# Kernel optimization log

Measured on AMD Instinct MI355X. Metric: run time of the kernel, lower is better.

The kernel has to match this reference:

```python
import jax
import jax.numpy as jnp
from jax import lax
import numpy as np

NUM_OUTPUT_POINTS = 2048
NUM_NEIGHBORS = 32


def setup_inputs() -> dict:
    key = jax.random.key(0)
    k1, k2 = jax.random.split(key)
    coordinates = jax.random.normal(k1, (8, 8192, 3), dtype=jnp.float32)
    features = jax.random.normal(k2, (8, 8192, 128), dtype=jnp.float32)
    return {"coordinates": coordinates, "features": features}


def farthest_point_sample(coords, num_output_points):
    """Deterministic FPS (first point = index 0). coords: (B, N, D) -> idx (B, M) int32."""
    B, N, D = coords.shape

    def step(carry, _):
        dist, farthest = carry  # (B, N), (B,)
        centroid = jnp.take_along_axis(coords, farthest[:, None, None], axis=1)  # (B,1,D)
        cur = jnp.linalg.norm(coords - centroid, axis=-1)  # (B, N), L2 norm
        dist = jnp.minimum(dist, cur)
        new_far = jnp.argmax(dist, axis=-1).astype(jnp.int32)
        return (dist, new_far), farthest

    init = (jnp.full((B, N), 1e10, coords.dtype), jnp.zeros((B,), jnp.int32))
    _, idx = lax.scan(step, init, None, length=num_output_points)  # (M, B)
    return idx.T  # (B, M)


def knn_point(num_neighbors, coords, centers):
    """coords (B,N,D), centers (B,M,D) -> (B,M,K) indices of nearest neighbors (L2)."""
    # squared distances via expansion (avoids (B,M,N,D) diff tensor)
    c2 = jnp.sum(centers * centers, axis=-1, keepdims=True)        # (B,M,1)
    p2 = jnp.sum(coords * coords, axis=-1)[:, None, :]             # (B,1,N)
    d2 = c2 + p2 - 2.0 * jnp.einsum('bmd,bnd->bmn', centers, coords)
    _, nbr_idx = lax.top_k(-d2, num_neighbors)                     # smallest distances
    return nbr_idx


def _gather_points(points, idx):
    """points (B,N,C), idx (B,...) -> (B,...,C)."""
    return jax.vmap(lambda p, i: p[i])(points, idx)


def reference(coordinates, features):
    fps_idx = farthest_point_sample(coordinates, NUM_OUTPUT_POINTS)      # (B, M)
    out_coordinates = _gather_points(coordinates, fps_idx)               # (B, M, D)
    nbr_idx = knn_point(NUM_NEIGHBORS, coordinates, out_coordinates)     # (B, M, K)
    group_features = _gather_points(features, nbr_idx)                   # (B, M, K, C)
    out_features = jnp.mean(group_features, axis=2)                      # (B, M, C)
    return out_coordinates, out_features
```

## Files before the change

### kernel.cpp

```cpp
#include <hip/hip_runtime.h>

typedef unsigned int u32;
typedef unsigned long long u64;
typedef float f32x2 __attribute__((ext_vector_type(2)));

#define BB 8
#define NN 8192
#define MM 2048
#define KK 32
#define CC 128

#define FPS_T 512
#define FPS_PAIRS 8

template <int Ctrl, int RowMask>
__device__ __forceinline__ int dpp_mov(int x) {
  return __builtin_amdgcn_update_dpp(x, x, Ctrl, RowMask, 0xf, false);
}
template <int Ctrl, int RowMask>
__device__ __forceinline__ u32 dpp_scan_add(u32 x) {
  return x + (u32)__builtin_amdgcn_update_dpp(0, (int)x, Ctrl, RowMask, 0xf, false);
}

__device__ __forceinline__ float wave_max63(float v) {
  v = fmaxf(v, __int_as_float(dpp_mov<0x111, 0xf>(__float_as_int(v))));
  v = fmaxf(v, __int_as_float(dpp_mov<0x112, 0xf>(__float_as_int(v))));
  v = fmaxf(v, __int_as_float(dpp_mov<0x114, 0xf>(__float_as_int(v))));
  v = fmaxf(v, __int_as_float(dpp_mov<0x118, 0xf>(__float_as_int(v))));
  v = fmaxf(v, __int_as_float(dpp_mov<0x142, 0xa>(__float_as_int(v))));
  v = fmaxf(v, __int_as_float(dpp_mov<0x143, 0xc>(__float_as_int(v))));
  return v;
}

__device__ __forceinline__ u32 wave_minu63(u32 v) {
  u32 o;
  o = (u32)dpp_mov<0x111, 0xf>((int)v); v = o < v ? o : v;
  o = (u32)dpp_mov<0x112, 0xf>((int)v); v = o < v ? o : v;
  o = (u32)dpp_mov<0x114, 0xf>((int)v); v = o < v ? o : v;
  o = (u32)dpp_mov<0x118, 0xf>((int)v); v = o < v ? o : v;
  o = (u32)dpp_mov<0x142, 0xa>((int)v); v = o < v ? o : v;
  o = (u32)dpp_mov<0x143, 0xc>((int)v); v = o < v ? o : v;
  return v;
}

__device__ __forceinline__ u32 wave_scan_incl(u32 x) {
  x = dpp_scan_add<0x111, 0xf>(x);
  x = dpp_scan_add<0x112, 0xf>(x);
  x = dpp_scan_add<0x114, 0xf>(x);
  x = dpp_scan_add<0x118, 0xf>(x);
  x = dpp_scan_add<0x142, 0xa>(x);
  x = dpp_scan_add<0x143, 0xc>(x);
  return x;
}

#define PK_ADD(d, a, b) asm("v_pk_add_f32 %0, %1, %2" : "=v"(d) : "v"(a), "v"(b))
#define PK_MUL(d, a, b) asm("v_pk_mul_f32 %0, %1, %2" : "=v"(d) : "v"(a), "v"(b))

__global__ __launch_bounds__(FPS_T, 1)
void fps_kernel(const float* __restrict__ coords, float* __restrict__ out_coords) {
  const int b = blockIdx.x;
  const int t = threadIdx.x;
  const float* cb = coords + (size_t)b * NN * 3;

  __shared__ float s_x[NN], s_y[NN], s_z[NN];
  __shared__ float s_gpart[FPS_T / 64];
  __shared__ u32 s_ipart[FPS_T / 64];

  f32x2 x[FPS_PAIRS], y[FPS_PAIRS], z[FPS_PAIRS], d2m[FPS_PAIRS];
#pragma unroll
  for (int k = 0; k < FPS_PAIRS; ++k) {
    const int p0 = t + (2 * k) * FPS_T;
    const int p1 = t + (2 * k + 1) * FPS_T;
    x[k].x = cb[p0 * 3 + 0]; x[k].y = cb[p1 * 3 + 0];
    y[k].x = cb[p0 * 3 + 1]; y[k].y = cb[p1 * 3 + 1];
    z[k].x = cb[p0 * 3 + 2]; z[k].y = cb[p1 * 3 + 2];
    d2m[k].x = 1e20f; d2m[k].y = 1e20f;
    s_x[p0] = x[k].x; s_x[p1] = x[k].y;
    s_y[p0] = y[k].x; s_y[p1] = y[k].y;
    s_z[p0] = z[k].x; s_z[p1] = z[k].y;
  }

  if (t == 0) {
    out_coords[(size_t)(b * MM) * 3 + 0] = cb[0];
    out_coords[(size_t)(b * MM) * 3 + 1] = cb[1];
    out_coords[(size_t)(b * MM) * 3 + 2] = cb[2];
  }
  float cx = cb[0], cy = cb[1], cz = cb[2];

  for (int it = 1; it < MM; ++it) {
    const f32x2 ncx = {-cx, -cx}, ncy = {-cy, -cy}, ncz = {-cz, -cz};
    f32x2 bv = {-1.0f, -1.0f};
#pragma unroll
    for (int k = 0; k < FPS_PAIRS; ++k) {
      f32x2 dx, dy, dz, t0, t1, t2, d2;
      PK_ADD(dx, x[k], ncx);
      PK_ADD(dy, y[k], ncy);
      PK_ADD(dz, z[k], ncz);
      PK_MUL(t0, dx, dx);
      PK_MUL(t1, dy, dy);
      PK_ADD(t0, t0, t1);
      PK_MUL(t2, dz, dz);
      PK_ADD(d2, t0, t2);
      d2m[k].x = fminf(d2m[k].x, d2.x);
      d2m[k].y = fminf(d2m[k].y, d2.y);
      bv.x = fmaxf(bv.x, d2m[k].x);
      bv.y = fmaxf(bv.y, d2m[k].y);
    }
    const float bestv = fmaxf(bv.x, bv.y);

    const float wv = wave_max63(bestv);
    if ((t & 63) == 63) s_gpart[t >> 6] = wv;
    __syncthreads();
    float gmax = s_gpart[0];
#pragma unroll
    for (int w = 1; w < FPS_T / 64; ++w) gmax = fmaxf(gmax, s_gpart[w]);

    float lo_f;
    if (!(gmax > 0.0f)) {
      lo_f = 0.0f;
    } else {
      const float s = __fsqrt_rn(gmax);
      const float sp = __int_as_float(__float_as_int(s) - 1);
      const double mid = 0.5 * ((double)s + (double)sp);
      const double lod = mid * mid;
      float c = (float)lod;
      if ((double)c < lod) c = __int_as_float(__float_as_int(c) + 1);
      lo_f = c;
    }

    u32 mi = 0xFFFFFFFFu;
    if (bestv >= lo_f) {
#pragma unroll
      for (int k = 0; k < FPS_PAIRS; ++k) {
        const u32 p0 = (u32)(t + (2 * k) * FPS_T);
        const u32 p1 = (u32)(t + (2 * k + 1) * FPS_T);
        if (d2m[k].x >= lo_f && p0 < mi) mi = p0;
        if (d2m[k].y >= lo_f && p1 < mi) mi = p1;
      }
    }
    const u32 wi = wave_minu63(mi);
    if ((t & 63) == 63) s_ipart[t >> 6] = wi;
    __syncthreads();
    u32 widx = s_ipart[0];
#pragma unroll
    for (int w = 1; w < FPS_T / 64; ++w)
      widx = s_ipart[w] < widx ? s_ipart[w] : widx;

    cx = s_x[widx]; cy = s_y[widx]; cz = s_z[widx];
    if (t == (it & (FPS_T - 1))) {
      float* oc = out_coords + ((size_t)b * MM + it) * 3;
      oc[0] = cx; oc[1] = cy; oc[2] = cz;
    }
  }
}

__global__ __launch_bounds__(256, 4)
void knn_mean_kernel(const float* __restrict__ coords,
                     const float* __restrict__ feats,
                     const float* __restrict__ out_coords,
                     float* __restrict__ out_feats) {
  const int q = blockIdx.x;
  const int b = q >> 11;
  const int t = threadIdx.x;
  const float* cb = coords + (size_t)b * NN * 3;

  const float cx = out_coords[(size_t)q * 3 + 0];
  const float cy = out_coords[(size_t)q * 3 + 1];
  const float cz = out_coords[(size_t)q * 3 + 2];
  const float c2 = __fadd_rn(__fadd_rn(__fmul_rn(cx, cx), __fmul_rn(cy, cy)),
                             __fmul_rn(cz, cz));

  u32 D[32];
  const float* tb = cb + t * 96;
#pragma unroll
  for (int ch = 0; ch < 8; ++ch) {
    const float4 q0 = *(const float4*)(tb + ch * 12 + 0);
    const float4 q1 = *(const float4*)(tb + ch * 12 + 4);
    const float4 q2 = *(const float4*)(tb + ch * 12 + 8);
    const float pxs[4] = {q0.x, q0.w, q1.z, q2.y};
    const float pys[4] = {q0.y, q1.x, q1.w, q2.z};
    const float pzs[4] = {q0.z, q1.y, q2.x, q2.w};
#pragma unroll
    for (int kk = 0; kk < 4; ++kk) {
      const int j = ch * 4 + kk;
      const float px = pxs[kk], py = pys[kk], pz = pzs[kk];
      const float p2 = __fadd_rn(__fadd_rn(__fmul_rn(px, px), __fmul_rn(py, py)),
                                 __fmul_rn(pz, pz));
      const float dot = __fmaf_rn(cz, pz, __fmaf_rn(cy, py, __fmul_rn(cx, px)));
      const float d2 = __fsub_rn(__fadd_rn(c2, p2), __fadd_rn(dot, dot));
      u32 ub = __float_as_uint(d2);
      ub ^= (((u32)((int)ub >> 31)) | 0x80000000u);
      D[j] = ub;
    }
  }

  __shared__ u32 s_hist[4096];
  __shared__ u32 s_wsum[4];
  __shared__ u32 s_bin, s_r, s_full;
  __shared__ u32 s_cnt;
  __shared__ int s_nbr[KK];
  __shared__ float s_sum[CC];

  const int w = t >> 6;
  u64 hi = 0;
  u32 k_rem = KK;
  u64 thr = 0;
  bool done = false;

  constexpr int SHIFT[4] = {33, 22, 11, 0};
  constexpr int SBITS[4] = {45, 33, 22, 11};

#pragma unroll
  for (int p = 0; p < 4; ++p) {
    if (!done) {
      const uint4 z4 = {0u, 0u, 0u, 0u};
#pragma unroll
      for (int i = 0; i < 4; ++i) *(uint4*)&s_hist[t * 16 + i * 4] = z4;
      __syncthreads();

#pragma unroll
      for (int j = 0; j < 32; ++j) {
        const u64 key = ((u64)D[j] << 13) | (u32)(t * 32 + j);
        if ((key >> SBITS[p]) == hi)
          atomicAdd(&s_hist[(u32)(key >> SHIFT[p]) & 4095u], 1u);
      }
      __syncthreads();

      const uint4 h0 = *(const uint4*)&s_hist[t * 16 + 0];
      const uint4 h1 = *(const uint4*)&s_hist[t * 16 + 4];
      const uint4 h2 = *(const uint4*)&s_hist[t * 16 + 8];
      const uint4 h3 = *(const uint4*)&s_hist[t * 16 + 12];
      const u32 ls = h0.x + h0.y + h0.z + h0.w + h1.x + h1.y + h1.z + h1.w +
                     h2.x + h2.y + h2.z + h2.w + h3.x + h3.y + h3.z + h3.w;
      const u32 incl = wave_scan_incl(ls);
      if ((t & 63) == 63) s_wsum[w] = incl;
      __syncthreads();
      u32 base = 0;
      if (w > 0) base += s_wsum[0];
      if (w > 1) base += s_wsum[1];
      if (w > 2) base += s_wsum[2];
      const u32 pre_grp = base + incl - ls;

      if (pre_grp < k_rem && k_rem <= pre_grp + ls) {
        const u32 hh[16] = {h0.x, h0.y, h0.z, h0.w, h1.x, h1.y, h1.z, h1.w,
                            h2.x, h2.y, h2.z, h2.w, h3.x, h3.y, h3.z, h3.w};
        u32 c = pre_grp;
#pragma unroll
        for (int i = 0; i < 16; ++i) {
          const u32 h = hh[i];
          if (k_rem > c && k_rem <= c + h) {
            s_bin = (u32)(t * 16 + i);
            s_r = k_rem - c;
            s_full = (k_rem - c == h) ? 1u : 0u;
          }
          c += h;
        }
      }
      __syncthreads();

      const u32 bin = s_bin;
      const u32 r = s_r;
      const u32 fullf = s_full;
      hi = (hi << (SBITS[p] - SHIFT[p])) | bin;
      if (fullf) {
        thr = (SHIFT[p] > 0)
                  ? ((hi << SHIFT[p]) | ((1ULL << SHIFT[p]) - 1ULL))
                  : hi;
        done = true;
      } else {
        k_rem = r;
      }
    }
  }

  if (t == 0) s_cnt = 0;
  __syncthreads();
#pragma unroll
  for (int j = 0; j < 32; ++j) {
    const u64 key = ((u64)D[j] << 13) | (u32)(t * 32 + j);
    if (key <= thr) {
      const u32 pos = atomicAdd(&s_cnt, 1u);
      s_nbr[pos] = t * 32 + j;
    }
  }
  __syncthreads();

  const int c = t & (CC - 1);
  const int half = t >> 7;
  const float* fb = feats + (size_t)b * NN * CC;
  float s = 0.0f;
#pragma unroll
  for (int k = 0; k < 16; ++k) {
    const int p = s_nbr[half * 16 + k];
    s = __fadd_rn(s, fb[(size_t)p * CC + c]);
  }
  if (half == 1) s_sum[c] = s;
  __syncthreads();
  if (half == 0) {
    const float tot = __fadd_rn(s, s_sum[c]);
    out_feats[(size_t)q * CC + c] = tot * 0.03125f;
  }
}

extern "C" void kernel_launch(void* const* d_in, const int* in_sizes, int n_in,
                              void* d_out, int out_size, void* d_ws, size_t ws_size,
                              hipStream_t stream) {
  const float* coords = (const float*)d_in[0];
  const float* feats  = (const float*)d_in[1];
  float* out_coords = (float*)d_out;
  float* out_feats  = (float*)d_out + (size_t)BB * MM * 3;

  fps_kernel<<<BB, FPS_T, 0, stream>>>(coords, out_coords);
  knn_mean_kernel<<<BB * MM, 256, 0, stream>>>(coords, feats, out_coords,
                                               out_feats);
}
```

Measured before the change: 2.499 ms.

## Spatially sort FPS points into Morton cells and skip threads/waves via bounding spheres

Before the FPS loop, the kernel bins each batch's points into a 16^3 Morton-ordered grid with a shared-memory histogram and prefix scan, so every thread holds 16 spatially adjacent points. It then builds a bounding sphere per thread and per wave. Each iteration tests the new centroid against these spheres, using conservative rounding factors, and skips the distance update when no point in the sphere can get a smaller min-distance. The argmax tie-break now compares square roots and uses the original point indices, meant to match the reference's L2-norm argmax. This adds setup cost and divergence, and exact equivalence depends on the rounding bounds.

```diff
diff --git a/kernel.cpp b/kernel.cpp
--- a/kernel.cpp
+++ b/kernel.cpp
@@ -2,7 +2,6 @@
 
 typedef unsigned int u32;
 typedef unsigned long long u64;
-typedef float f32x2 __attribute__((ext_vector_type(2)));
 
 #define BB 8
 #define NN 8192
@@ -11,7 +10,11 @@
 #define CC 128
 
 #define FPS_T 512
-#define FPS_PAIRS 8
+#define FPS_P 16
+#define NCELL 4096
+
+#define C_DOWN 0.9999961853027344f
+#define C_UP   1.0000038146972656f
 
 template <int Ctrl, int RowMask>
 __device__ __forceinline__ int dpp_mov(int x) {
@@ -31,7 +34,15 @@
   v = fmaxf(v, __int_as_float(dpp_mov<0x143, 0xc>(__float_as_int(v))));
   return v;
 }
-
+__device__ __forceinline__ float wave_min63f(float v) {
+  v = fminf(v, __int_as_float(dpp_mov<0x111, 0xf>(__float_as_int(v))));
+  v = fminf(v, __int_as_float(dpp_mov<0x112, 0xf>(__float_as_int(v))));
+  v = fminf(v, __int_as_float(dpp_mov<0x114, 0xf>(__float_as_int(v))));
+  v = fminf(v, __int_as_float(dpp_mov<0x118, 0xf>(__float_as_int(v))));
+  v = fminf(v, __int_as_float(dpp_mov<0x142, 0xa>(__float_as_int(v))));
+  v = fminf(v, __int_as_float(dpp_mov<0x143, 0xc>(__float_as_int(v))));
+  return v;
+}
 __device__ __forceinline__ u32 wave_minu63(u32 v) {
   u32 o;
   o = (u32)dpp_mov<0x111, 0xf>((int)v); v = o < v ? o : v;
@@ -42,7 +53,6 @@
   o = (u32)dpp_mov<0x143, 0xc>((int)v); v = o < v ? o : v;
   return v;
 }
-
 __device__ __forceinline__ u32 wave_scan_incl(u32 x) {
   x = dpp_scan_add<0x111, 0xf>(x);
   x = dpp_scan_add<0x112, 0xf>(x);
@@ -52,32 +62,106 @@
   x = dpp_scan_add<0x143, 0xc>(x);
   return x;
 }
-
-#define PK_ADD(d, a, b) asm("v_pk_add_f32 %0, %1, %2" : "=v"(d) : "v"(a), "v"(b))
-#define PK_MUL(d, a, b) asm("v_pk_mul_f32 %0, %1, %2" : "=v"(d) : "v"(a), "v"(b))
+__device__ __forceinline__ float rl63(float v) {
+  return __uint_as_float((u32)__builtin_amdgcn_readlane(__float_as_int(v), 63));
+}
+
+__device__ __forceinline__ u32 spread4(u32 a) {
+  return (a & 1u) | ((a & 2u) << 2) | ((a & 4u) << 4) | ((a & 8u) << 6);
+}
+__device__ __forceinline__ u32 cell_of(float x, float y, float z) {
+  const u32 qx = (u32)(int)fminf(fmaxf((x + 6.0f) * 1.3333334f, 0.0f), 15.0f);
+  const u32 qy = (u32)(int)fminf(fmaxf((y + 6.0f) * 1.3333334f, 0.0f), 15.0f);
+  const u32 qz = (u32)(int)fminf(fmaxf((z + 6.0f) * 1.3333334f, 0.0f), 15.0f);
+  return spread4(qx) | (spread4(qy) << 1) | (spread4(qz) << 2);
+}
 
 __global__ __launch_bounds__(FPS_T, 1)
 void fps_kernel(const float* __restrict__ coords, float* __restrict__ out_coords) {
-  const int b = blockIdx.x;
-  const int t = threadIdx.x;
+  const int b = blockIdx.x, t = threadIdx.x, w = t >> 6, lane = t & 63;
   const float* cb = coords + (size_t)b * NN * 3;
 
   __shared__ float s_x[NN], s_y[NN], s_z[NN];
+  __shared__ u32 s_sidx[NN];
+  __shared__ u32 s_hist[NCELL];
   __shared__ float s_gpart[FPS_T / 64];
   __shared__ u32 s_ipart[FPS_T / 64];
-
-  f32x2 x[FPS_PAIRS], y[FPS_PAIRS], z[FPS_PAIRS], d2m[FPS_PAIRS];
-#pragma unroll
-  for (int k = 0; k < FPS_PAIRS; ++k) {
-    const int p0 = t + (2 * k) * FPS_T;
-    const int p1 = t + (2 * k + 1) * FPS_T;
-    x[k].x = cb[p0 * 3 + 0]; x[k].y = cb[p1 * 3 + 0];
-    y[k].x = cb[p0 * 3 + 1]; y[k].y = cb[p1 * 3 + 1];
-    z[k].x = cb[p0 * 3 + 2]; z[k].y = cb[p1 * 3 + 2];
-    d2m[k].x = 1e20f; d2m[k].y = 1e20f;
-    s_x[p0] = x[k].x; s_x[p1] = x[k].y;
-    s_y[p0] = y[k].x; s_y[p1] = y[k].y;
-    s_z[p0] = z[k].x; s_z[p1] = z[k].y;
+  __shared__ u32 s_wsum[FPS_T / 64];
+
+  u32 cell[FPS_P];
+  {
+    float lx[FPS_P], ly[FPS_P], lz[FPS_P];
+#pragma unroll
+    for (int j = 0; j < FPS_P; ++j) {
+      const int p = t + j * FPS_T;
+      lx[j] = cb[p * 3 + 0]; ly[j] = cb[p * 3 + 1]; lz[j] = cb[p * 3 + 2];
+      s_x[p] = lx[j]; s_y[p] = ly[j]; s_z[p] = lz[j];
+    }
+#pragma unroll
+    for (int i = 0; i < NCELL / FPS_T; ++i) s_hist[t + i * FPS_T] = 0u;
+    __syncthreads();
+#pragma unroll
+    for (int j = 0; j < FPS_P; ++j) {
+      cell[j] = cell_of(lx[j], ly[j], lz[j]);
+      atomicAdd(&s_hist[cell[j]], 1u);
+    }
+  }
+  __syncthreads();
+
+  {
+    u32 h[8], ls = 0;
+#pragma unroll
+    for (int i = 0; i < 8; ++i) { h[i] = s_hist[t * 8 + i]; ls += h[i]; }
+    const u32 incl = wave_scan_incl(ls);
+    if (lane == 63) s_wsum[w] = incl;
+    __syncthreads();
+    u32 base = 0;
+#pragma unroll
+    for (int w2 = 0; w2 < FPS_T / 64; ++w2) base += (w2 < w) ? s_wsum[w2] : 0u;
+    u32 run = base + incl - ls;
+#pragma unroll
+    for (int i = 0; i < 8; ++i) { const u32 hv = h[i]; s_hist[t * 8 + i] = run; run += hv; }
+  }
+  __syncthreads();
+
+#pragma unroll
+  for (int j = 0; j < FPS_P; ++j) {
+    const u32 pos = atomicAdd(&s_hist[cell[j]], 1u);
+    s_sidx[pos] = (u32)(t + j * FPS_T);
+  }
+  __syncthreads();
+
+  float x[FPS_P], y[FPS_P], z[FPS_P], d2m[FPS_P];
+  u32 idx[FPS_P];
+  float ccx, ccy, ccz, Rup;
+  {
+    float sx = 0.f, sy = 0.f, sz = 0.f;
+#pragma unroll
+    for (int j = 0; j < FPS_P; ++j) {
+      idx[j] = s_sidx[t * FPS_P + j];
+      x[j] = s_x[idx[j]]; y[j] = s_y[idx[j]]; z[j] = s_z[idx[j]];
+      d2m[j] = 1e20f;
+      sx += x[j]; sy += y[j]; sz += z[j];
+    }
+    ccx = sx * 0.0625f; ccy = sy * 0.0625f; ccz = sz * 0.0625f;
+    float r2 = 0.f;
+#pragma unroll
+    for (int j = 0; j < FPS_P; ++j) {
+      const float dx = x[j] - ccx, dy = y[j] - ccy, dz = z[j] - ccz;
+      r2 = fmaxf(r2, dx * dx + dy * dy + dz * dz);
+    }
+    Rup = __fsqrt_rn(r2) * C_UP + 1e-30f;
+  }
+
+  float wcx, wcy, wcz, wR;
+  {
+    const float lx = rl63(wave_min63f(ccx - Rup)), hx = rl63(wave_max63(ccx + Rup));
+    const float ly = rl63(wave_min63f(ccy - Rup)), hy = rl63(wave_max63(ccy + Rup));
+    const float lz = rl63(wave_min63f(ccz - Rup)), hz = rl63(wave_max63(ccz + Rup));
+    wcx = (lx + hx) * 0.5f; wcy = (ly + hy) * 0.5f; wcz = (lz + hz) * 0.5f;
+    const float ddx = ccx - wcx, ddy = ccy - wcy, ddz = ccz - wcz;
+    const float dr = __fsqrt_rn(ddx * ddx + ddy * ddy + ddz * ddz) * C_UP + Rup;
+    wR = rl63(wave_max63(dr)) * C_UP + 1e-30f;
   }
 
   if (t == 0) {
@@ -86,65 +170,63 @@
     out_coords[(size_t)(b * MM) * 3 + 2] = cb[2];
   }
   float cx = cb[0], cy = cb[1], cz = cb[2];
+  float bestv = 1e20f;
+  float wbest = 1e20f;
 
   for (int it = 1; it < MM; ++it) {
-    const f32x2 ncx = {-cx, -cx}, ncy = {-cy, -cy}, ncz = {-cz, -cz};
-    f32x2 bv = {-1.0f, -1.0f};
-#pragma unroll
-    for (int k = 0; k < FPS_PAIRS; ++k) {
-      f32x2 dx, dy, dz, t0, t1, t2, d2;
-      PK_ADD(dx, x[k], ncx);
-      PK_ADD(dy, y[k], ncy);
-      PK_ADD(dz, z[k], ncz);
-      PK_MUL(t0, dx, dx);
-      PK_MUL(t1, dy, dy);
-      PK_ADD(t0, t0, t1);
-      PK_MUL(t2, dz, dz);
-      PK_ADD(d2, t0, t2);
-      d2m[k].x = fminf(d2m[k].x, d2.x);
-      d2m[k].y = fminf(d2m[k].y, d2.y);
-      bv.x = fmaxf(bv.x, d2m[k].x);
-      bv.y = fmaxf(bv.y, d2m[k].y);
-    }
-    const float bestv = fmaxf(bv.x, bv.y);
-
-    const float wv = wave_max63(bestv);
-    if ((t & 63) == 63) s_gpart[t >> 6] = wv;
+    const float wdx = __fsub_rn(wcx, cx), wdy = __fsub_rn(wcy, cy), wdz = __fsub_rn(wcz, cz);
+    const float wd2 = __fadd_rn(__fadd_rn(__fmul_rn(wdx, wdx), __fmul_rn(wdy, wdy)),
+                                __fmul_rn(wdz, wdz));
+    const float wlc = __fsub_rn(__fmul_rn(__fsqrt_rn(wd2), C_DOWN), wR);
+    const bool wskip = (wlc > 0.0f) &&
+                       (__fmul_rn(__fmul_rn(wlc, wlc), C_DOWN) >= wbest);
+    if (!wskip) {
+      const float tdx = __fsub_rn(ccx, cx), tdy = __fsub_rn(ccy, cy), tdz = __fsub_rn(ccz, cz);
+      const float td2 = __fadd_rn(__fadd_rn(__fmul_rn(tdx, tdx), __fmul_rn(tdy, tdy)),
+                                  __fmul_rn(tdz, tdz));
+      const float tlc = __fsub_rn(__fmul_rn(__fsqrt_rn(td2), C_DOWN), Rup);
+      const bool tskip = (tlc > 0.0f) &&
+                         (__fmul_rn(__fmul_rn(tlc, tlc), C_DOWN) >= bestv);
+      if (!tskip) {
+        float bv = -1.0f;
+#pragma unroll
+        for (int j = 0; j < FPS_P; ++j) {
+          const float dx = __fsub_rn(x[j], cx);
+          const float dy = __fsub_rn(y[j], cy);
+          const float dz = __fsub_rn(z[j], cz);
+          const float d2 = __fadd_rn(__fadd_rn(__fmul_rn(dx, dx), __fmul_rn(dy, dy)),
+                                     __fmul_rn(dz, dz));
+          const float nd = fminf(d2m[j], d2);
+          d2m[j] = nd;
+          bv = fmaxf(bv, nd);
+        }
+        bestv = bv;
+      }
+      const float wv = wave_max63(bestv);
+      if (lane == 63) s_gpart[w] = wv;
+      wbest = rl63(wv);
+    } else {
+      if (lane == 63) s_gpart[w] = wbest;
+    }
     __syncthreads();
     float gmax = s_gpart[0];
 #pragma unroll
-    for (int w = 1; w < FPS_T / 64; ++w) gmax = fmaxf(gmax, s_gpart[w]);
-
-    float lo_f;
-    if (!(gmax > 0.0f)) {
-      lo_f = 0.0f;
-    } else {
-      const float s = __fsqrt_rn(gmax);
-      const float sp = __int_as_float(__float_as_int(s) - 1);
-      const double mid = 0.5 * ((double)s + (double)sp);
-      const double lod = mid * mid;
-      float c = (float)lod;
-      if ((double)c < lod) c = __int_as_float(__float_as_int(c) + 1);
-      lo_f = c;
-    }
+    for (int w2 = 1; w2 < FPS_T / 64; ++w2) gmax = fmaxf(gmax, s_gpart[w2]);
+    const float s = __fsqrt_rn(gmax);
 
     u32 mi = 0xFFFFFFFFu;
-    if (bestv >= lo_f) {
-#pragma unroll
-      for (int k = 0; k < FPS_PAIRS; ++k) {
-        const u32 p0 = (u32)(t + (2 * k) * FPS_T);
-        const u32 p1 = (u32)(t + (2 * k + 1) * FPS_T);
-        if (d2m[k].x >= lo_f && p0 < mi) mi = p0;
-        if (d2m[k].y >= lo_f && p1 < mi) mi = p1;
-      }
+    if (__fsqrt_rn(bestv) == s) {
+#pragma unroll
+      for (int j = 0; j < FPS_P; ++j)
+        if (__fsqrt_rn(d2m[j]) == s && idx[j] < mi) mi = idx[j];
     }
     const u32 wi = wave_minu63(mi);
-    if ((t & 63) == 63) s_ipart[t >> 6] = wi;
+    if (lane == 63) s_ipart[w] = wi;
     __syncthreads();
     u32 widx = s_ipart[0];
 #pragma unroll
-    for (int w = 1; w < FPS_T / 64; ++w)
-      widx = s_ipart[w] < widx ? s_ipart[w] : widx;
+    for (int w2 = 1; w2 < FPS_T / 64; ++w2)
+      widx = s_ipart[w2] < widx ? s_ipart[w2] : widx;
 
     cx = s_x[widx]; cy = s_y[widx]; cz = s_z[widx];
     if (t == (it & (FPS_T - 1))) {
@@ -263,9 +345,8 @@
       const u32 fullf = s_full;
       hi = (hi << (SBITS[p] - SHIFT[p])) | bin;
       if (fullf) {
-        thr = (SHIFT[p] > 0)
-                  ? ((hi << SHIFT[p]) | ((1ULL << SHIFT[p]) - 1ULL))
-                  : hi;
+        thr = (SHIFT[p] > 0) ? ((hi << SHIFT[p]) | ((1ULL << SHIFT[p]) - 1ULL))
+                             : hi;
         done = true;
       } else {
         k_rem = r;
```

After: 3.289 ms. 1.32x slower.
